# Optimization experiments

Hardware: AMD Instinct MI355X
Metric: run time of the kernel (lower is better)

Reference implementation:

```python
import jax, jax.numpy as jnp
import numpy as np

D_MODEL = 1024
N_HEADS = 16
D_K = D_MODEL // N_HEADS
NEG = -1e9


def setup_inputs() -> dict:
    key = jax.random.key(0)
    ks = jax.random.split(key, 6)
    B, T, D = 4, 2048, D_MODEL
    s = 1.0 / np.sqrt(D)
    x = jax.random.normal(ks[0], (B, T, D), dtype=jnp.float32)
    Wq = jax.random.normal(ks[1], (D, D), dtype=jnp.float32) * s
    Wk = jax.random.normal(ks[2], (D, D), dtype=jnp.float32) * s
    Wv = jax.random.normal(ks[3], (D, D), dtype=jnp.float32) * s
    Wo = jax.random.normal(ks[4], (D, D), dtype=jnp.float32) * s
    bo = jnp.zeros((D,), dtype=jnp.float32)
    # causal mask: True above diagonal = masked (masked_fill where True)
    mask = jnp.triu(jnp.ones((T, T), dtype=bool), k=1)
    return {"x": x, "mask": mask, "Wq": Wq, "Wk": Wk, "Wv": Wv, "Wo": Wo, "bo": bo}


def reference(x, mask, Wq, Wk, Wv, Wo, bo):
    B, T, D = x.shape
    # torch nn.Linear: y = x @ W.T
    q = (x @ Wq.T).reshape(B, T, N_HEADS, D_K).transpose(0, 2, 1, 3)  # [B,H,T,dk]
    k = (x @ Wk.T).reshape(B, T, N_HEADS, D_K).transpose(0, 2, 1, 3)
    v = (x @ Wv.T).reshape(B, T, N_HEADS, D_K).transpose(0, 2, 1, 3)
    scores = jnp.einsum("bhqd,bhkd->bhqk", q, k) / np.sqrt(D_K)  # [B,H,T,T]
    scores = jnp.where(mask[:T, :T], NEG, scores)
    attn = jax.nn.softmax(scores, axis=-1)
    ctx = jnp.einsum("bhqk,bhkd->bhqd", attn, v)  # [B,H,T,dk]
    ctx = ctx.transpose(0, 2, 1, 3).reshape(B, T, D)
    return ctx @ Wo.T + bo
```

## Files before the change

kernel.cpp:

```cpp
#include <hip/hip_runtime.h>
#include <hip/hip_bf16.h>


typedef __attribute__((ext_vector_type(8))) short bf16x8;
typedef __attribute__((ext_vector_type(4))) float f32x4;

__device__ __forceinline__ unsigned short f2b(float x) {
  __hip_bfloat16 h = __float2bfloat16(x);
  return __builtin_bit_cast(unsigned short, h);
}

__device__ __forceinline__ void load_lds16(const void* g, void* l) {
  __builtin_amdgcn_global_load_lds((__attribute__((address_space(1))) void*)g,
                                   (__attribute__((address_space(3))) void*)l,
                                   16, 0, 0);
}

__global__ void cast_kernel(const float* __restrict__ x,
                            const float* __restrict__ w0, const float* __restrict__ w1,
                            const float* __restrict__ w2, const float* __restrict__ w3,
                            unsigned short* __restrict__ xb, unsigned short* __restrict__ wb) {
  int i = blockIdx.x * 256 + threadIdx.x;
  const float* src;
  unsigned short* dst;
  int c;
  if (i < 1048576) {
    src = x; dst = xb; c = i;
  } else {
    int cw = i - 1048576;
    int wi = cw >> 17;
    c = cw & 131071;
    src = (wi == 0) ? w0 : (wi == 1) ? w1 : (wi == 2) ? w2 : w3;
    dst = wb + ((size_t)wi << 20);
  }
  const float4* s4 = (const float4*)src;
  float4 a = s4[2 * c], b = s4[2 * c + 1];
  union { unsigned short u[8]; uint4 v; } r;
  r.u[0] = f2b(a.x); r.u[1] = f2b(a.y); r.u[2] = f2b(a.z); r.u[3] = f2b(a.w);
  r.u[4] = f2b(b.x); r.u[5] = f2b(b.y); r.u[6] = f2b(b.z); r.u[7] = f2b(b.w);
  ((uint4*)dst)[c] = r.v;
}

__launch_bounds__(256)
__global__ void gemm_bt(const unsigned short* __restrict__ A,
                        const unsigned short* __restrict__ Bw,
                        void* __restrict__ Cout,
                        const float* __restrict__ bias,
                        int mode) {
  __shared__ unsigned short At[128 * 64];
  __shared__ unsigned short Bt[128 * 64];

  const int tid = threadIdx.x;
  const int lane = tid & 63;
  const int w = tid >> 6;
  const int quad = lane >> 4;
  const int l15 = lane & 15;
  const int m0 = blockIdx.x * 128;
  const int n0 = blockIdx.y * 128;
  const int wm = (w >> 1) * 64;
  const int wn = (w & 1) * 64;

  const f32x4 z4 = {0.f, 0.f, 0.f, 0.f};
  f32x4 acc[4][4];
#pragma unroll
  for (int i = 0; i < 4; ++i)
#pragma unroll
    for (int j = 0; j < 4; ++j) acc[i][j] = z4;

  for (int kt = 0; kt < 1024; kt += 64) {
    __syncthreads();
#pragma unroll
    for (int c = 0; c < 4; ++c) {
      int chunk = c * 256 + tid;
      int row = chunk >> 3;
      int scol = (chunk & 7) ^ (row & 7);
      load_lds16(A + (size_t)(m0 + row) * 1024 + kt + scol * 8,
                 &At[((c * 256 + (w << 6)) << 3)]);
      load_lds16(Bw + (size_t)(n0 + row) * 1024 + kt + scol * 8,
                 &Bt[((c * 256 + (w << 6)) << 3)]);
    }
    __syncthreads();
#pragma unroll
    for (int ks = 0; ks < 2; ++ks) {
      bf16x8 af[4], bf[4];
#pragma unroll
      for (int i = 0; i < 4; ++i) {
        int rowA = wm + i * 16 + l15;
        af[i] = *(const bf16x8*)&At[rowA * 64 + (((ks * 4 + quad) ^ (rowA & 7)) << 3)];
        int rowB = wn + i * 16 + l15;
        bf[i] = *(const bf16x8*)&Bt[rowB * 64 + (((ks * 4 + quad) ^ (rowB & 7)) << 3)];
      }
#pragma unroll
      for (int i = 0; i < 4; ++i)
#pragma unroll
        for (int j = 0; j < 4; ++j)
          acc[i][j] = __builtin_amdgcn_mfma_f32_16x16x32_bf16(af[i], bf[j], acc[i][j], 0, 0, 0);
    }
  }

  const int seg = n0 >> 10;
#pragma unroll
  for (int i = 0; i < 4; ++i) {
#pragma unroll
    for (int j = 0; j < 4; ++j) {
#pragma unroll
      for (int r = 0; r < 4; ++r) {
        int m = m0 + wm + i * 16 + quad * 4 + r;
        int n = n0 + wn + j * 16 + l15;
        float v = acc[i][j][r];
        if (mode == 1) {
          int nn = n & 1023;
          unsigned short* base = (unsigned short*)Cout;
          if (seg == 0) {
            base[(size_t)m * 1024 + nn] = f2b(v);
          } else if (seg == 1) {
            (base + 8388608)[(size_t)m * 1024 + nn] = f2b(v);
          } else {
            int b = m >> 11, t = m & 2047, h = nn >> 6, d = nn & 63;
            (base + 16777216)[(((size_t)((b * 16 + h) * 64 + d)) << 11) + t] = f2b(v);
          }
        } else {
          ((float*)Cout)[(size_t)m * 1024 + n] = v + bias[n];
        }
      }
    }
  }
}

__launch_bounds__(256)
__global__ void attn_kernel(const unsigned short* __restrict__ Q,
                            const unsigned short* __restrict__ K,
                            const unsigned short* __restrict__ VT,
                            unsigned short* __restrict__ ctx) {
  __shared__ unsigned short Kt[2][64 * 64];
  __shared__ unsigned short Vt[2][64 * 64];
  __shared__ unsigned short Pt[64 * 64];

  const int tid = threadIdx.x;
  const int lane = tid & 63;
  const int w = tid >> 6;
  const int quad = lane >> 4;
  const int l15 = lane & 15;
  const int p = blockIdx.x;
  const int bh = blockIdx.y;
  const int b = bh >> 4, h = bh & 15;

  const unsigned short* Kg = K + ((size_t)(b * 2048)) * 1024 + h * 64;
  const unsigned short* Vg = VT + ((size_t)bh * 64) * 2048;

  const float SC = 0.1803368801f;
  const float M0 = 11.0f;

  for (int tt = 0; tt < 2; ++tt) {
    const int qt = tt ? (31 - p) : p;
    const int qb = qt * 64;

    const unsigned short* qbase =
        Q + ((size_t)(b * 2048 + qb + w * 16 + l15)) * 1024 + h * 64;
    bf16x8 qa[2];
    qa[0] = *(const bf16x8*)(qbase + quad * 8);
    qa[1] = *(const bf16x8*)(qbase + 32 + quad * 8);

    const f32x4 z4 = {0.f, 0.f, 0.f, 0.f};
    f32x4 o[4];
#pragma unroll
    for (int nt = 0; nt < 4; ++nt) o[nt] = z4;
    float lrow = 0.f;

    if (tt) __syncthreads();

#pragma unroll
    for (int c = 0; c < 2; ++c) {
      int chunk = c * 256 + tid;
      int row = chunk >> 3;
      int scol = (chunk & 7) ^ (row & 7);
      load_lds16(Kg + (size_t)row * 1024 + scol * 8, &Kt[0][((c * 256 + (w << 6)) << 3)]);
      load_lds16(Vg + ((size_t)row << 11) + scol * 8, &Vt[0][((c * 256 + (w << 6)) << 3)]);
    }

    int cur = 0;
    for (int j = 0; j <= qt; ++j) {
      const int j0 = j * 64;
      __syncthreads();

      if (j < qt) {
        const int nj0 = j0 + 64;
#pragma unroll
        for (int c = 0; c < 2; ++c) {
          int chunk = c * 256 + tid;
          int row = chunk >> 3;
          int scol = (chunk & 7) ^ (row & 7);
          load_lds16(Kg + (size_t)(nj0 + row) * 1024 + scol * 8,
                     &Kt[cur ^ 1][((c * 256 + (w << 6)) << 3)]);
          load_lds16(Vg + ((size_t)row << 11) + nj0 + scol * 8,
                     &Vt[cur ^ 1][((c * 256 + (w << 6)) << 3)]);
        }
      }

      f32x4 st[4];
#pragma unroll
      for (int nt = 0; nt < 4; ++nt) st[nt] = z4;
#pragma unroll
      for (int ks = 0; ks < 2; ++ks) {
#pragma unroll
        for (int nt = 0; nt < 4; ++nt) {
          int rowK = nt * 16 + l15;
          bf16x8 kf = *(const bf16x8*)&Kt[cur][rowK * 64 + (((ks * 4 + quad) ^ (rowK & 7)) << 3)];
          st[nt] = __builtin_amdgcn_mfma_f32_16x16x32_bf16(kf, qa[ks], st[nt], 0, 0, 0);
        }
      }

      const bool diag = (j == qt);
      const int q = qb + w * 16 + l15;
      float sum = 0.f;
#pragma unroll
      for (int nt = 0; nt < 4; ++nt) {
#pragma unroll
        for (int r = 0; r < 4; ++r) {
          float e = fmaf(st[nt][r], SC, -M0);
          if (diag) {
            int kpos = j0 + nt * 16 + quad * 4 + r;
            if (kpos > q) e = -1e30f;
          }
          float pv = exp2f(e);
          st[nt][r] = pv;
          sum += pv;
        }
      }
      sum += __shfl_xor(sum, 16);
      sum += __shfl_xor(sum, 32);
      lrow += sum;

      const int qrow = w * 16 + l15;
#pragma unroll
      for (int nt = 0; nt < 4; ++nt) {
        ushort4 pk;
        pk.x = f2b(st[nt][0]); pk.y = f2b(st[nt][1]);
        pk.z = f2b(st[nt][2]); pk.w = f2b(st[nt][3]);
        int chunk = nt * 4 + quad;
        *(ushort4*)&Pt[qrow * 64 + ((chunk ^ l15) << 2)] = pk;
      }

#pragma unroll
      for (int ks = 0; ks < 2; ++ks) {
        int c0 = ks * 8 + quad * 2;
        union { ushort4 hh[2]; bf16x8 v; } pu;
        pu.hh[0] = *(const ushort4*)&Pt[qrow * 64 + ((c0 ^ l15) << 2)];
        pu.hh[1] = *(const ushort4*)&Pt[qrow * 64 + (((c0 + 1) ^ l15) << 2)];
#pragma unroll
        for (int nt = 0; nt < 4; ++nt) {
          int rowV = nt * 16 + l15;
          bf16x8 vb = *(const bf16x8*)&Vt[cur][rowV * 64 + (((ks * 4 + quad) ^ (rowV & 7)) << 3)];
          o[nt] = __builtin_amdgcn_mfma_f32_16x16x32_bf16(pu.v, vb, o[nt], 0, 0, 0);
        }
      }
      cur ^= 1;
    }

    float lf[4];
#pragma unroll
    for (int r = 0; r < 4; ++r) lf[r] = 1.f / __shfl(lrow, quad * 4 + r);
#pragma unroll
    for (int nt = 0; nt < 4; ++nt) {
#pragma unroll
      for (int r = 0; r < 4; ++r) {
        int q = qb + w * 16 + quad * 4 + r;
        int dcol = nt * 16 + l15;
        ctx[((size_t)(b * 2048 + q)) * 1024 + h * 64 + dcol] = f2b(o[nt][r] * lf[r]);
      }
    }
  }
}

extern "C" void kernel_launch(void* const* d_in, const int* in_sizes, int n_in,
                              void* d_out, int out_size, void* d_ws, size_t ws_size,
                              hipStream_t stream) {
  const float* x  = (const float*)d_in[0];
  const float* Wq = (const float*)d_in[2];
  const float* Wk = (const float*)d_in[3];
  const float* Wv = (const float*)d_in[4];
  const float* Wo = (const float*)d_in[5];
  const float* bo = (const float*)d_in[6];
  float* out = (float*)d_out;

  unsigned short* xb  = (unsigned short*)d_ws;
  unsigned short* wb  = xb + 8388608;
  unsigned short* Qb  = wb + 4 * 1048576;
  unsigned short* Kb  = Qb + 8388608;
  unsigned short* VTb = Kb + 8388608;
  unsigned short* ctxb = xb;

  cast_kernel<<<6144, 256, 0, stream>>>(x, Wq, Wk, Wv, Wo, xb, wb);

  gemm_bt<<<dim3(64, 24), 256, 0, stream>>>(xb, wb, Qb, nullptr, 1);

  attn_kernel<<<dim3(16, 64), 256, 0, stream>>>(Qb, Kb, VTb, ctxb);

  gemm_bt<<<dim3(64, 8), 256, 0, stream>>>(ctxb, wb + 3 * 1048576, out, bo, 3);
}
```

Baseline: 304.4 us.

## Enlarge QKV GEMM tiles and split-K the output projection with atomics

The QKV projection GEMM now uses 256x128 tiles, with each wave computing 128x64, so every B fragment is reused across more MFMA work and fewer blocks are launched. The output projection is split along K into two halves. Partial sums are added into the fp32 output with atomicAdd, after a new bias_init kernel pre-fills the output with the bias. This trades the QKV GEMM's register pressure and occupancy for data reuse. It also adds atomic traffic and an extra kernel launch to raise parallelism in the small final GEMM.

Result: slower. 375.7 us (+23.4%).

```diff
diff --git a/kernel.cpp b/kernel.cpp
--- a/kernel.cpp
+++ b/kernel.cpp
@@ -41,12 +41,103 @@
   ((uint4*)dst)[c] = r.v;
 }
 
+__global__ void bias_init(const float* __restrict__ bias, float* __restrict__ out) {
+  int i = blockIdx.x * 256 + threadIdx.x;
+  ((float4*)out)[i] = ((const float4*)bias)[i & 255];
+}
+
 __launch_bounds__(256)
-__global__ void gemm_bt(const unsigned short* __restrict__ A,
-                        const unsigned short* __restrict__ Bw,
-                        void* __restrict__ Cout,
-                        const float* __restrict__ bias,
-                        int mode) {
+__global__ void gemm_qkv(const unsigned short* __restrict__ A,
+                         const unsigned short* __restrict__ Bw,
+                         unsigned short* __restrict__ Cout) {
+  __shared__ unsigned short At[256 * 64];
+  __shared__ unsigned short Bt[128 * 64];
+
+  const int tid = threadIdx.x;
+  const int lane = tid & 63;
+  const int w = tid >> 6;
+  const int quad = lane >> 4;
+  const int l15 = lane & 15;
+  const int m0 = blockIdx.x * 256;
+  const int n0 = blockIdx.y * 128;
+  const int wm = (w >> 1) * 128;
+  const int wn = (w & 1) * 64;
+
+  const f32x4 z4 = {0.f, 0.f, 0.f, 0.f};
+  f32x4 acc[8][4];
+#pragma unroll
+  for (int i = 0; i < 8; ++i)
+#pragma unroll
+    for (int j = 0; j < 4; ++j) acc[i][j] = z4;
+
+  for (int kt = 0; kt < 1024; kt += 64) {
+    __syncthreads();
+#pragma unroll
+    for (int c = 0; c < 8; ++c) {
+      int chunk = c * 256 + tid;
+      int row = chunk >> 3;
+      int scol = (chunk & 7) ^ (row & 7);
+      load_lds16(A + (size_t)(m0 + row) * 1024 + kt + scol * 8,
+                 &At[((c * 256 + (w << 6)) << 3)]);
+    }
+#pragma unroll
+    for (int c = 0; c < 4; ++c) {
+      int chunk = c * 256 + tid;
+      int row = chunk >> 3;
+      int scol = (chunk & 7) ^ (row & 7);
+      load_lds16(Bw + (size_t)(n0 + row) * 1024 + kt + scol * 8,
+                 &Bt[((c * 256 + (w << 6)) << 3)]);
+    }
+    __syncthreads();
+#pragma unroll
+    for (int ks = 0; ks < 2; ++ks) {
+      bf16x8 af[8], bf[4];
+#pragma unroll
+      for (int i = 0; i < 8; ++i) {
+        int rowA = wm + i * 16 + l15;
+        af[i] = *(const bf16x8*)&At[rowA * 64 + (((ks * 4 + quad) ^ (rowA & 7)) << 3)];
+      }
+#pragma unroll
+      for (int j = 0; j < 4; ++j) {
+        int rowB = wn + j * 16 + l15;
+        bf[j] = *(const bf16x8*)&Bt[rowB * 64 + (((ks * 4 + quad) ^ (rowB & 7)) << 3)];
+      }
+#pragma unroll
+      for (int i = 0; i < 8; ++i)
+#pragma unroll
+        for (int j = 0; j < 4; ++j)
+          acc[i][j] = __builtin_amdgcn_mfma_f32_16x16x32_bf16(af[i], bf[j], acc[i][j], 0, 0, 0);
+    }
+  }
+
+  const int seg = n0 >> 10;
+#pragma unroll
+  for (int i = 0; i < 8; ++i) {
+#pragma unroll
+    for (int j = 0; j < 4; ++j) {
+#pragma unroll
+      for (int r = 0; r < 4; ++r) {
+        int m = m0 + wm + i * 16 + quad * 4 + r;
+        int n = n0 + wn + j * 16 + l15;
+        int nn = n & 1023;
+        float v = acc[i][j][r];
+        if (seg == 0) {
+          Cout[(size_t)m * 1024 + nn] = f2b(v);
+        } else if (seg == 1) {
+          (Cout + 8388608)[(size_t)m * 1024 + nn] = f2b(v);
+        } else {
+          int b = m >> 11, t = m & 2047, h = nn >> 6, d = nn & 63;
+          (Cout + 16777216)[(((size_t)((b * 16 + h) * 64 + d)) << 11) + t] = f2b(v);
+        }
+      }
+    }
+  }
+}
+
+__launch_bounds__(256)
+__global__ void gemm_proj(const unsigned short* __restrict__ A,
+                          const unsigned short* __restrict__ Bw,
+                          float* __restrict__ out) {
   __shared__ unsigned short At[128 * 64];
   __shared__ unsigned short Bt[128 * 64];
 
@@ -57,6 +148,7 @@
   const int l15 = lane & 15;
   const int m0 = blockIdx.x * 128;
   const int n0 = blockIdx.y * 128;
+  const int kbase = blockIdx.z * 512;
   const int wm = (w >> 1) * 64;
   const int wn = (w & 1) * 64;
 
@@ -67,7 +159,7 @@
 #pragma unroll
     for (int j = 0; j < 4; ++j) acc[i][j] = z4;
 
-  for (int kt = 0; kt < 1024; kt += 64) {
+  for (int kt = kbase; kt < kbase + 512; kt += 64) {
     __syncthreads();
 #pragma unroll
     for (int c = 0; c < 4; ++c) {
@@ -98,33 +190,16 @@
     }
   }
 
-  const int seg = n0 >> 10;
-#pragma unroll
-  for (int i = 0; i < 4; ++i) {
-#pragma unroll
-    for (int j = 0; j < 4; ++j) {
+#pragma unroll
+  for (int i = 0; i < 4; ++i)
+#pragma unroll
+    for (int j = 0; j < 4; ++j)
 #pragma unroll
       for (int r = 0; r < 4; ++r) {
         int m = m0 + wm + i * 16 + quad * 4 + r;
         int n = n0 + wn + j * 16 + l15;
-        float v = acc[i][j][r];
-        if (mode == 1) {
-          int nn = n & 1023;
-          unsigned short* base = (unsigned short*)Cout;
-          if (seg == 0) {
-            base[(size_t)m * 1024 + nn] = f2b(v);
-          } else if (seg == 1) {
-            (base + 8388608)[(size_t)m * 1024 + nn] = f2b(v);
-          } else {
-            int b = m >> 11, t = m & 2047, h = nn >> 6, d = nn & 63;
-            (base + 16777216)[(((size_t)((b * 16 + h) * 64 + d)) << 11) + t] = f2b(v);
-          }
-        } else {
-          ((float*)Cout)[(size_t)m * 1024 + n] = v + bias[n];
-        }
-      }
-    }
-  }
+        atomicAdd(&out[(size_t)m * 1024 + n], acc[i][j][r]);
+      }
 }
 
 __launch_bounds__(256)
@@ -291,10 +366,11 @@
   unsigned short* ctxb = xb;
 
   cast_kernel<<<6144, 256, 0, stream>>>(x, Wq, Wk, Wv, Wo, xb, wb);
-
-  gemm_bt<<<dim3(64, 24), 256, 0, stream>>>(xb, wb, Qb, nullptr, 1);
+  bias_init<<<8192, 256, 0, stream>>>(bo, out);
+
+  gemm_qkv<<<dim3(32, 24), 256, 0, stream>>>(xb, wb, Qb);
 
   attn_kernel<<<dim3(16, 64), 256, 0, stream>>>(Qb, Kb, VTb, ctxb);
 
-  gemm_bt<<<dim3(64, 8), 256, 0, stream>>>(ctxb, wb + 3 * 1048576, out, bo, 3);
-}
+  gemm_proj<<<dim3(64, 8, 2), 256, 0, stream>>>(ctxb, wb + 3 * 1048576, out);
+}
```
